# Kernel optimization log

Hardware: AMD Instinct MI355X
Metric: run time of the kernel (lower is better)

## Reference

```python
import jax, jax.numpy as jnp
import numpy as np

B, L = 4, 40960
C = 512
DMLP = 2048
TEMP = 1e-5
EPS = 1e-5
FACTOR = 2  # Smartpool factor at layer 4


def setup_inputs() -> dict:
    key = jax.random.key(0)
    ks = jax.random.split(key, 8)

    def w(k, shape, fan_in):
        return jax.random.normal(k, shape, jnp.float32) / np.float32(np.sqrt(fan_in))

    inp = {
        "x": jax.random.normal(ks[0], (B, 1, L), jnp.float32),
        "conv0_w": w(ks[1], (C, 1, 10), 10),   "conv0_b": jnp.zeros(C, jnp.float32),
        "conv1_w": w(ks[2], (C, C, 8), C * 8), "conv1_b": jnp.zeros(C, jnp.float32),
        "conv2_w": w(ks[3], (C, C, 4), C * 4), "conv2_b": jnp.zeros(C, jnp.float32),
        "conv3_w": w(ks[4], (C, C, 4), C * 4), "conv3_b": jnp.zeros(C, jnp.float32),
        "mlp_w1": w(ks[5], (C, DMLP), C),       "mlp_b1": jnp.zeros(DMLP, jnp.float32),
        "mlp_w2": w(ks[6], (DMLP, DMLP), DMLP), "mlp_b2": jnp.zeros(DMLP, jnp.float32),
        "mlp_w3": w(ks[7], (DMLP, 1), DMLP),    "mlp_b3": jnp.zeros(1, jnp.float32),
    }
    for i in range(5):  # ChannelNorm affine params (init: ones/zeros)
        inp[f"n{i}_w"] = jnp.ones(C, jnp.float32)
        inp[f"n{i}_b"] = jnp.zeros(C, jnp.float32)
    return inp


def _conv(x, w, b, stride, pad):
    # Conv1d with padding_mode='reflect': reflect-pad then VALID conv. x: [B,C,T]
    x = jnp.pad(x, ((0, 0), (0, 0), (pad, pad)), mode="reflect")
    y = jax.lax.conv_general_dilated(x, w, (stride,), "VALID",
                                     dimension_numbers=("NCH", "OIH", "NCH"))
    return y + b[None, :, None]


def _cnorm(x, g, b):
    # ChannelNorm: normalize over channel dim with unbiased variance (torch.var default)
    m = jnp.mean(x, axis=1, keepdims=True)
    v = jnp.var(x, axis=1, keepdims=True, ddof=1)
    return (x - m) * jax.lax.rsqrt(v + EPS) * g[None, :, None] + b[None, :, None]


def _forward(x, conv0_w, conv0_b, conv1_w, conv1_b, conv2_w, conv2_b, conv3_w, conv3_b,
             n0_w, n0_b, n1_w, n1_b, n2_w, n2_b, n3_w, n3_b, n4_w, n4_b,
             mlp_w1, mlp_b1, mlp_w2, mlp_b2, mlp_w3, mlp_b3):
    h = jax.nn.relu(_cnorm(_conv(x, conv0_w, conv0_b, 5, 3), n0_w, n0_b))
    h = jax.nn.relu(_cnorm(_conv(h, conv1_w, conv1_b, 4, 2), n1_w, n1_b))
    h = jax.nn.relu(_cnorm(_conv(h, conv2_w, conv2_b, 2, 1), n2_w, n2_b))
    h = jax.nn.relu(_cnorm(_conv(h, conv3_w, conv3_b, 2, 1), n3_w, n3_b))

    f = jnp.transpose(h, (0, 2, 1))  # [B,T,C]
    T = f.shape[1]

    # importance MLP (dropout inactive in eval), exact GELU, sigmoid head
    z = jax.nn.gelu(f @ mlp_w1 + mlp_b1, approximate=False)
    z = jax.nn.gelu(z @ mlp_w2 + mlp_b2, approximate=False)
    imp = jax.nn.sigmoid((z @ mlp_w3 + mlp_b3)[..., 0]) + TEMP          # [B,T]
    imp = imp / jnp.sum(imp, axis=1, keepdims=True) * (T / FACTOR)      # sums to T/factor

    # warp: cumsum -> ramp contributions -> 2x2 [[-1,1],[1,-1]] conv = double diff
    Tn = T // FACTOR  # == round(importance_cs[0,-1])
    cs = jnp.cumsum(imp, axis=1)                                        # [B,T]
    p = jnp.maximum(cs[:, :, None] - jnp.arange(Tn, dtype=cs.dtype)[None, None, :], 0.0)  # [B,T,Tn]
    pc = jnp.pad(p, ((0, 0), (0, 0), (0, 1)))
    d = pc[:, :, :-1] - pc[:, :, 1:]                                    # diff along new-time axis
    wmat = d - jnp.pad(d, ((0, 0), (1, 0), (0, 0)))[:, :-1, :]          # diff along old-time axis, [B,T,Tn]
    pooled = jnp.einsum("btn,btc->bnc", wmat, f)                        # interp_weights @ X

    out = jnp.transpose(pooled, (0, 2, 1))                              # [B,C,Tn]
    return jax.nn.relu(_cnorm(out, n4_w, n4_b))


def reference(x, conv0_w, conv0_b, conv1_w, conv1_b, conv2_w, conv2_b, conv3_w, conv3_b,
              n0_w, n0_b, n1_w, n1_b, n2_w, n2_b, n3_w, n3_b, n4_w, n4_b,
              mlp_w1, mlp_b1, mlp_w2, mlp_b2, mlp_w3, mlp_b3):
    return _forward(x, conv0_w, conv0_b, conv1_w, conv1_b, conv2_w, conv2_b, conv3_w, conv3_b,
                    n0_w, n0_b, n1_w, n1_b, n2_w, n2_b, n3_w, n3_b, n4_w, n4_b,
                    mlp_w1, mlp_b1, mlp_w2, mlp_b2, mlp_w3, mlp_b3)
```

## Files before the change

kernel.cpp:

```cpp
#include <hip/hip_runtime.h>
#include <hip/hip_bf16.h>
#include <math.h>

#define NB 4
#define LIN 40960
#define NC 512
#define T0 8192
#define T1 2048
#define T2 1024
#define T3 512
#define TN 256
#define DM 2048
#define EPSF 1e-5f
#define TEMPF 1e-5f

typedef __attribute__((ext_vector_type(8))) short bf16x8;
typedef __attribute__((ext_vector_type(4))) float f32x4;

__device__ __forceinline__ int refl(int t, int T) {
  if (t < 0) t = -t;
  if (t >= T) t = 2 * T - 2 - t;
  return t;
}

__device__ __forceinline__ void gld16(void* lds, const void* g) {
  __builtin_amdgcn_global_load_lds((const __attribute__((address_space(1))) unsigned int*)g,
                                   (__attribute__((address_space(3))) unsigned int*)lds, 16, 0, 0);
}

__device__ __forceinline__ void blk_sum2_512(float& a, float& b, float* scratch) {
#pragma unroll
  for (int off = 32; off > 0; off >>= 1) {
    a += __shfl_down(a, off, 64);
    b += __shfl_down(b, off, 64);
  }
  int lane = threadIdx.x & 63, wid = threadIdx.x >> 6;
  __syncthreads();
  if (lane == 0) { scratch[wid] = a; scratch[8 + wid] = b; }
  __syncthreads();
  float sa = 0.f, sb = 0.f;
#pragma unroll
  for (int i = 0; i < 8; i++) { sa += scratch[i]; sb += scratch[8 + i]; }
  a = sa; b = sb;
}

__device__ __forceinline__ void add_bf8(const __hip_bfloat16* p, float* v) {
  union { uint4 u; __hip_bfloat16 h[8]; } pk;
  pk.u = *(const uint4*)p;
#pragma unroll
  for (int j = 0; j < 8; j++) v[j] += __bfloat162float(pk.h[j]);
}

template <int KT>
__device__ __forceinline__ void prep_conv_body(const float* __restrict__ w, __hip_bfloat16* __restrict__ wt,
                                               int co, float* l) {
  const float* wb = w + (size_t)co * 512 * KT;
  for (int i = threadIdx.x; i < 512 * KT; i += 512) l[i] = wb[i];
  __syncthreads();
  __hip_bfloat16* wo = wt + (size_t)co * 512 * KT;
  for (int i = threadIdx.x; i < 512 * KT; i += 512) {
    int kk = i >> 9, ci = i & 511;
    wo[i] = __float2bfloat16(l[ci * KT + kk]);
  }
}

template <int KD, int ND>
__device__ __forceinline__ void prep_mlp_body(const float* __restrict__ w, __hip_bfloat16* __restrict__ wt,
                                              int bidx, float* sbuf) {
  float(*tile)[33] = (float(*)[33])sbuf;
  int bx = bidx % (ND / 32);
  int by = bidx / (ND / 32);
  int tx = threadIdx.x & 31, ty = threadIdx.x >> 5;
#pragma unroll
  for (int i = 0; i < 32; i += 16)
    tile[ty + i][tx] = w[(size_t)(by * 32 + ty + i) * ND + bx * 32 + tx];
  __syncthreads();
#pragma unroll
  for (int i = 0; i < 32; i += 16)
    wt[(size_t)(bx * 32 + ty + i) * KD + by * 32 + tx] = __float2bfloat16(tile[tx][ty + i]);
}

__device__ __forceinline__ void conv0_body(const float* __restrict__ x, const float* __restrict__ w,
                                           const float* __restrict__ bias, const float* __restrict__ gw,
                                           const float* __restrict__ gb, __hip_bfloat16* __restrict__ out,
                                           int blk, float* smem) {
  float* xv = smem;
  float* tb = smem + 64;
  float* stats = smem + 4672;
  int b = blk / (T0 / 8);
  int t0 = (blk % (T0 / 8)) * 8;
  int tid = threadIdx.x;
  if (tid < 45) xv[tid] = x[(size_t)b * LIN + refl(t0 * 5 - 3 + tid, LIN)];
  __syncthreads();
  float wk[10];
#pragma unroll
  for (int k = 0; k < 10; k++) wk[k] = w[tid * 10 + k];
  float bs = bias[tid];
  float acc[8];
#pragma unroll
  for (int tt = 0; tt < 8; tt++) {
    float a = bs;
#pragma unroll
    for (int k = 0; k < 10; k++) a += xv[tt * 5 + k] * wk[k];
    acc[tt] = a;
    tb[tid * 9 + tt] = a;
  }
  __syncthreads();
  int wave = tid >> 6, lane = tid & 63;
  float s = 0.f, q = 0.f;
#pragma unroll
  for (int j = 0; j < 8; j++) {
    float v = tb[(lane * 8 + j) * 9 + wave];
    s += v; q += v * v;
  }
#pragma unroll
  for (int off = 32; off > 0; off >>= 1) {
    s += __shfl_xor(s, off, 64);
    q += __shfl_xor(q, off, 64);
  }
  if (lane == 0) {
    float mean = s * (1.f / NC);
    float var = fmaxf((q - s * s * (1.f / NC)) * (1.f / (NC - 1)), 0.f);
    stats[wave] = mean;
    stats[8 + wave] = rsqrtf(var + EPSF);
  }
  __syncthreads();
  float gwv = gw[tid], gbv = gb[tid];
#pragma unroll
  for (int tt = 0; tt < 8; tt++) {
    float y = (acc[tt] - stats[tt]) * stats[8 + tt] * gwv + gbv;
    out[((size_t)(b * T0 + t0 + tt)) * NC + tid] = __float2bfloat16(fmaxf(y, 0.f));
  }
}

__global__ __launch_bounds__(512) void k_init(const float* x, const float* c0w, const float* c0b,
                                              const float* n0w, const float* n0b, __hip_bfloat16* h0b,
                                              const float* c1w, const float* c2w, const float* c3w,
                                              const float* mw1, const float* mw2,
                                              __hip_bfloat16* wt1, __hip_bfloat16* wt2,
                                              __hip_bfloat16* wt3, __hip_bfloat16* wm1t,
                                              __hip_bfloat16* wm2t) {
  __shared__ float smem[4688];
  int b = blockIdx.x;
  if (b < 4096) conv0_body(x, c0w, c0b, n0w, n0b, h0b, b, smem);
  else if (b < 4608) prep_conv_body<8>(c1w, wt1, b - 4096, smem);
  else if (b < 5120) prep_conv_body<4>(c2w, wt2, b - 4608, smem);
  else if (b < 5632) prep_conv_body<4>(c3w, wt3, b - 5120, smem);
  else if (b < 6656) prep_mlp_body<512, 2048>(mw1, wm1t, b - 5632, smem);
  else prep_mlp_body<2048, 2048>(mw2, wm2t, b - 6656, smem);
}

template <int MODE, int TIN_, int TOUT_, int SS, int PP, int KK, int NN, int SPLITK, int MM>
__global__ __launch_bounds__(512, 2) void k_gemmE(const __hip_bfloat16* __restrict__ A,
                                                  const __hip_bfloat16* __restrict__ Bt,
                                                  __hip_bfloat16* __restrict__ Cp) {
  __shared__ __align__(16) __hip_bfloat16 sA[2][2][256 * 32];
  __shared__ __align__(16) __hip_bfloat16 sB[2][2][256 * 32];
  const int tid = threadIdx.x;
  const int lane = tid & 63;
  const int wave = tid >> 6;
  const int wm = wave >> 2, wn = wave & 3;
  constexpr int nt = NN / 256;
  constexpr int PS = (MM / 2048) * nt;
  constexpr int KBT = KK / 32;
  constexpr int NT = KBT / (2 * SPLITK);
  const int blk = blockIdx.x;
  const int xs = blk & 7, sl = blk >> 3;
  const int sk = sl / PS, rem = sl % PS;
  const int row0 = ((rem / nt) * 8 + xs) * 256;
  const int col0 = (rem % nt) * 256;
  const int kb0 = sk * (KBT / SPLITK);
  const int cq = lane >> 4, cl = lane & 15;

  const char* aP[2];
  const char* bP[2];

  auto stageA = [&](int kb, int buf, int kk) {
    bool recalc = (kb == kb0) || (MODE == 1 && (kb & 15) == 0);
    if (recalc) {
#pragma unroll
      for (int rr = 0; rr < 2; rr++) {
        int c = rr * 512 + tid;
        int m = c >> 2, kc = c & 3;
        int kcs = kc ^ (m & 3);
        size_t ga;
        if (MODE == 0) {
          ga = (size_t)(row0 + m) * KK + kb * 32 + kcs * 8;
        } else {
          int r = row0 + m;
          int bb = r / TOUT_;
          int t = r - bb * TOUT_;
          int k = (kb * 32) >> 9;
          int ci = ((kb * 32) & 511) + kcs * 8;
          int gt = refl(t * SS - PP + k, TIN_);
          ga = (((size_t)(bb * TIN_ + gt)) << 9) + ci;
        }
        aP[rr] = (const char*)(A + ga);
      }
    }
#pragma unroll
    for (int rr = 0; rr < 2; rr++) {
      gld16((char*)&sA[buf][kk][0] + (rr * 512 + tid) * 16, aP[rr]);
      aP[rr] += 64;
    }
  };

  auto stageB = [&](int buf, int kk) {
#pragma unroll
    for (int rr = 0; rr < 2; rr++) {
      gld16((char*)&sB[buf][kk][0] + (rr * 512 + tid) * 16, bP[rr]);
      bP[rr] += 64;
    }
  };

#pragma unroll
  for (int rr = 0; rr < 2; rr++) {
    int c = rr * 512 + tid;
    int n = c >> 2, kc = c & 3;
    int kcs = kc ^ (n & 3);
    bP[rr] = (const char*)(Bt + (size_t)(col0 + n) * KK + kb0 * 32 + kcs * 8);
  }

  f32x4 acc[8][4];
  const f32x4 zz = {0.f, 0.f, 0.f, 0.f};
#pragma unroll
  for (int mi = 0; mi < 8; mi++)
#pragma unroll
    for (int ni = 0; ni < 4; ni++) acc[mi][ni] = zz;

  stageA(kb0, 0, 0);
  stageB(0, 0);
  stageA(kb0 + 1, 0, 1);
  stageB(0, 1);
  asm volatile("s_waitcnt vmcnt(0)" ::: "memory");
  __builtin_amdgcn_s_barrier();

  const int p = cq ^ (cl & 3);
  for (int t = 0; t < NT; ++t) {
    const int buf = t & 1;
    const int kbase = kb0 + 2 * t;
    const short* bA0 = (const short*)&sA[buf][0][0];
    const short* bA1 = (const short*)&sA[buf][1][0];
    const short* bB0 = (const short*)&sB[buf][0][0];
    const short* bB1 = (const short*)&sB[buf][1][0];
    bf16x8 bfr0[4], bfr1[4];
#pragma unroll
    for (int q = 0; q < 4; ++q) {
      bf16x8 af0[2], af1[2];
      if (q == 0) {
#pragma unroll
        for (int ni = 0; ni < 4; ni++) {
          bfr0[ni] = *(const bf16x8*)(bB0 + (wn * 64 + ni * 16 + cl) * 32 + p * 8);
          bfr1[ni] = *(const bf16x8*)(bB1 + (wn * 64 + ni * 16 + cl) * 32 + p * 8);
        }
      }
#pragma unroll
      for (int i = 0; i < 2; i++) {
        int mi = q * 2 + i;
        af0[i] = *(const bf16x8*)(bA0 + (wm * 128 + mi * 16 + cl) * 32 + p * 8);
        af1[i] = *(const bf16x8*)(bA1 + (wm * 128 + mi * 16 + cl) * 32 + p * 8);
      }
      if (t + 1 < NT) {
        if (q == 0) stageA(kbase + 2, buf ^ 1, 0);
        else if (q == 1) stageB(buf ^ 1, 0);
        else if (q == 2) stageA(kbase + 3, buf ^ 1, 1);
        else stageB(buf ^ 1, 1);
      }
      __builtin_amdgcn_s_barrier();
      asm volatile("s_waitcnt lgkmcnt(0)" ::: "memory");
      __builtin_amdgcn_s_setprio(1);
#pragma unroll
      for (int i = 0; i < 2; i++)
#pragma unroll
        for (int ni = 0; ni < 4; ni++) {
          acc[q * 2 + i][ni] =
              __builtin_amdgcn_mfma_f32_16x16x32_bf16(af0[i], bfr0[ni], acc[q * 2 + i][ni], 0, 0, 0);
          acc[q * 2 + i][ni] =
              __builtin_amdgcn_mfma_f32_16x16x32_bf16(af1[i], bfr1[ni], acc[q * 2 + i][ni], 0, 0, 0);
        }
      __builtin_amdgcn_s_setprio(0);
      if (q == 3 && t + 1 < NT) asm volatile("s_waitcnt vmcnt(0)" ::: "memory");
      __builtin_amdgcn_s_barrier();
    }
  }

#pragma unroll
  for (int mi = 0; mi < 8; mi++)
#pragma unroll
    for (int ni = 0; ni < 4; ni++)
#pragma unroll
      for (int r2 = 0; r2 < 4; r2++) {
        int row = row0 + wm * 128 + mi * 16 + cq * 4 + r2;
        int col = col0 + wn * 64 + ni * 16 + cl;
        Cp[(size_t)sk * MM * NN + (size_t)row * NN + col] = __float2bfloat16(acc[mi][ni][r2]);
      }
}

template <int MODE, int TIN_, int TOUT_, int SS, int PP, int KK, int NN, int SPLITK, int MM>
__global__ __launch_bounds__(256) void k_gemmB(const __hip_bfloat16* __restrict__ A,
                                               const __hip_bfloat16* __restrict__ Bt,
                                               __hip_bfloat16* __restrict__ Cp) {
  __shared__ __align__(16) __hip_bfloat16 sA[2][128 * 32];
  __shared__ __align__(16) __hip_bfloat16 sB[2][2][128 * 32];
  const int tid = threadIdx.x;
  const int lane = tid & 63;
  const int wave = tid >> 6;
  const int wm = wave >> 1, wn = wave & 1;
  constexpr int nt = NN / 128;
  constexpr int PS = (MM / 1024) * nt;
  constexpr int KBT = KK / 32;
  const int blk = blockIdx.x;
  const int xs = blk & 7, sl = blk >> 3;
  const int sk = sl / PS, rem = sl % PS;
  const int row0 = ((rem / nt) * 8 + xs) * 128;
  const int col0 = (rem % nt) * 128;
  const int kb0 = (sk * KBT) / SPLITK, kb1 = ((sk + 1) * KBT) / SPLITK;
  const int cq = lane >> 4, cl = lane & 15;

  const char* aP[2];
  const char* bP[2];

  auto stageA = [&](int kb, int buf) {
    bool recalc = (kb == kb0) || (MODE == 1 && (kb & 15) == 0);
    if (recalc) {
#pragma unroll
      for (int rr = 0; rr < 2; rr++) {
        int c = rr * 256 + tid;
        int m = c >> 2, kc = c & 3;
        int kcs = kc ^ (m & 3);
        size_t ga;
        if (MODE == 0) {
          ga = (size_t)(row0 + m) * KK + kb * 32 + kcs * 8;
        } else {
          int r = row0 + m;
          int bb = r / TOUT_;
          int t = r - bb * TOUT_;
          int k = (kb * 32) >> 9;
          int ci = ((kb * 32) & 511) + kcs * 8;
          int gt = refl(t * SS - PP + k, TIN_);
          ga = (((size_t)(bb * TIN_ + gt)) << 9) + ci;
        }
        aP[rr] = (const char*)(A + ga);
      }
    }
#pragma unroll
    for (int rr = 0; rr < 2; rr++) {
      gld16((char*)&sA[buf][0] + (rr * 256 + tid) * 16, aP[rr]);
      aP[rr] += 64;
    }
  };

  auto stageB = [&](int buf, bool doSub1) {
#pragma unroll
    for (int rr = 0; rr < 2; rr++) {
      gld16((char*)&sB[buf][0][0] + (rr * 256 + tid) * 16, bP[rr]);
      if (doSub1) gld16((char*)&sB[buf][1][0] + (rr * 256 + tid) * 16, bP[rr] + 64);
      bP[rr] += 128;
    }
  };

#pragma unroll
  for (int rr = 0; rr < 2; rr++) {
    int c = rr * 256 + tid;
    int n = c >> 2, kc = c & 3;
    int kcs = kc ^ (n & 3);
    bP[rr] = (const char*)(Bt + (size_t)(col0 + n) * KK + kb0 * 32 + kcs * 8);
  }

  f32x4 acc[4][4];
  const f32x4 zz = {0.f, 0.f, 0.f, 0.f};
#pragma unroll
  for (int mi = 0; mi < 4; mi++)
#pragma unroll
    for (int ni = 0; ni < 4; ni++) acc[mi][ni] = zz;

  stageA(kb0, 0);
  stageB(0, kb0 + 1 < kb1);

  const int p = cq ^ (cl & 3);
  for (int kb = kb0; kb < kb1; kb++) {
    const int jj = kb - kb0;
    __syncthreads();
    if (kb + 1 < kb1) stageA(kb + 1, (jj + 1) & 1);
    if (((jj & 1) == 0) && (kb + 2 < kb1)) stageB(((jj >> 1) + 1) & 1, kb + 3 < kb1);
    const short* bA = (const short*)&sA[jj & 1][0];
    const short* bB = (const short*)&sB[(jj >> 1) & 1][jj & 1][0];
    bf16x8 af[4], bfr[4];
#pragma unroll
    for (int mi = 0; mi < 4; mi++)
      af[mi] = *(const bf16x8*)(bA + (wm * 64 + mi * 16 + cl) * 32 + p * 8);
#pragma unroll
    for (int ni = 0; ni < 4; ni++)
      bfr[ni] = *(const bf16x8*)(bB + (wn * 64 + ni * 16 + cl) * 32 + p * 8);
#pragma unroll
    for (int mi = 0; mi < 4; mi++)
#pragma unroll
      for (int ni = 0; ni < 4; ni++)
        acc[mi][ni] = __builtin_amdgcn_mfma_f32_16x16x32_bf16(af[mi], bfr[ni], acc[mi][ni], 0, 0, 0);
  }

#pragma unroll
  for (int mi = 0; mi < 4; mi++)
#pragma unroll
    for (int ni = 0; ni < 4; ni++)
#pragma unroll
      for (int r2 = 0; r2 < 4; r2++) {
        int row = row0 + wm * 64 + mi * 16 + cq * 4 + r2;
        int col = col0 + wn * 64 + ni * 16 + cl;
        Cp[(size_t)sk * MM * NN + (size_t)row * NN + col] = __float2bfloat16(acc[mi][ni][r2]);
      }
}

template <int MODE, int TIN_, int TOUT_, int SS, int PP, int KK, int NN, int EPI, int SPLITK, int MM>
__global__ __launch_bounds__(256, 4) void k_gemmC(const __hip_bfloat16* __restrict__ A,
                                                  const __hip_bfloat16* __restrict__ Bt,
                                                  const float* __restrict__ bias,
                                                  __hip_bfloat16* __restrict__ Cout) {
  __shared__ __align__(16) __hip_bfloat16 sA[2][64 * 32];
  __shared__ __align__(16) __hip_bfloat16 sB[2][2][128 * 32];
  const int tid = threadIdx.x;
  const int lane = tid & 63;
  const int wave = tid >> 6;
  const int wm = wave >> 1, wn = wave & 1;
  constexpr int nt = NN / 128;
  constexpr int PS = (MM / 512) * nt;
  constexpr int KBT = KK / 32;
  const int blk = blockIdx.x;
  const int xs = blk & 7, sl = blk >> 3;
  const int sk = sl / PS, rem = sl % PS;
  const int row0 = ((rem / nt) * 8 + xs) * 64;
  const int col0 = (rem % nt) * 128;
  const int kb0 = (sk * KBT) / SPLITK, kb1 = ((sk + 1) * KBT) / SPLITK;
  const int cq = lane >> 4, cl = lane & 15;

  const char* aP;
  const char* bP[2];

  auto stageA = [&](int kb, int buf) {
    bool recalc = (kb == kb0) || (MODE == 1 && (kb & 15) == 0);
    if (recalc) {
      int m = tid >> 2, kc = tid & 3;
      int kcs = kc ^ (m & 3);
      size_t ga;
      if (MODE == 0) {
        ga = (size_t)(row0 + m) * KK + kb * 32 + kcs * 8;
      } else {
        int r = row0 + m;
        int bb = r / TOUT_;
        int t = r - bb * TOUT_;
        int k = (kb * 32) >> 9;
        int ci = ((kb * 32) & 511) + kcs * 8;
        int gt = refl(t * SS - PP + k, TIN_);
        ga = (((size_t)(bb * TIN_ + gt)) << 9) + ci;
      }
      aP = (const char*)(A + ga);
    }
    gld16((char*)&sA[buf][0] + tid * 16, aP);
    aP += 64;
  };

  auto stageB = [&](int buf, bool doSub1) {
#pragma unroll
    for (int rr = 0; rr < 2; rr++) {
      gld16((char*)&sB[buf][0][0] + (rr * 256 + tid) * 16, bP[rr]);
      if (doSub1) gld16((char*)&sB[buf][1][0] + (rr * 256 + tid) * 16, bP[rr] + 64);
      bP[rr] += 128;
    }
  };

#pragma unroll
  for (int rr = 0; rr < 2; rr++) {
    int c = rr * 256 + tid;
    int n = c >> 2, kc = c & 3;
    int kcs = kc ^ (n & 3);
    bP[rr] = (const char*)(Bt + (size_t)(col0 + n) * KK + kb0 * 32 + kcs * 8);
  }

  f32x4 acc[2][4];
  const f32x4 zz = {0.f, 0.f, 0.f, 0.f};
#pragma unroll
  for (int mi = 0; mi < 2; mi++)
#pragma unroll
    for (int ni = 0; ni < 4; ni++) acc[mi][ni] = zz;

  stageA(kb0, 0);
  stageB(0, kb0 + 1 < kb1);

  const int p = cq ^ (cl & 3);
  for (int kb = kb0; kb < kb1; kb++) {
    const int jj = kb - kb0;
    __syncthreads();
    if (kb + 1 < kb1) stageA(kb + 1, (jj + 1) & 1);
    if (((jj & 1) == 0) && (kb + 2 < kb1)) stageB(((jj >> 1) + 1) & 1, kb + 3 < kb1);
    const short* bA = (const short*)&sA[jj & 1][0];
    const short* bB = (const short*)&sB[(jj >> 1) & 1][jj & 1][0];
    bf16x8 af[2], bfr[4];
#pragma unroll
    for (int mi = 0; mi < 2; mi++)
      af[mi] = *(const bf16x8*)(bA + (wm * 32 + mi * 16 + cl) * 32 + p * 8);
#pragma unroll
    for (int ni = 0; ni < 4; ni++)
      bfr[ni] = *(const bf16x8*)(bB + (wn * 64 + ni * 16 + cl) * 32 + p * 8);
#pragma unroll
    for (int mi = 0; mi < 2; mi++)
#pragma unroll
      for (int ni = 0; ni < 4; ni++)
        acc[mi][ni] = __builtin_amdgcn_mfma_f32_16x16x32_bf16(af[mi], bfr[ni], acc[mi][ni], 0, 0, 0);
  }

#pragma unroll
  for (int mi = 0; mi < 2; mi++)
#pragma unroll
    for (int ni = 0; ni < 4; ni++)
#pragma unroll
      for (int r2 = 0; r2 < 4; r2++) {
        int row = row0 + wm * 32 + mi * 16 + cq * 4 + r2;
        int col = col0 + wn * 64 + ni * 16 + cl;
        float v = acc[mi][ni][r2];
        if (EPI == 1) {
          v += bias[col];
          v = 0.5f * v * (1.f + erff(v * 0.70710678118654752f));
          Cout[(size_t)row * NN + col] = __float2bfloat16(v);
        } else {
          Cout[(size_t)sk * MM * NN + (size_t)row * NN + col] = __float2bfloat16(v);
        }
      }
}

template <int NS>
__global__ __launch_bounds__(512) void k_cnorm(const __hip_bfloat16* __restrict__ g,
                                               const float* __restrict__ cb,
                                               const float* __restrict__ gw, const float* __restrict__ gb,
                                               __hip_bfloat16* __restrict__ out, size_t stride) {
  int wave = threadIdx.x >> 6, lane = threadIdx.x & 63;
  size_t row = (size_t)blockIdx.x * 8 + wave;
  float v[8];
  {
    float4 c0 = *(const float4*)(cb + lane * 8), c1 = *(const float4*)(cb + lane * 8 + 4);
    v[0] = c0.x; v[1] = c0.y; v[2] = c0.z; v[3] = c0.w;
    v[4] = c1.x; v[5] = c1.y; v[6] = c1.z; v[7] = c1.w;
  }
#pragma unroll
  for (int s = 0; s < NS; s++) add_bf8(g + s * stride + row * NC + lane * 8, v);
  float s = 0.f, q = 0.f;
#pragma unroll
  for (int j = 0; j < 8; j++) { s += v[j]; q += v[j] * v[j]; }
#pragma unroll
  for (int off = 32; off > 0; off >>= 1) {
    s += __shfl_xor(s, off, 64);
    q += __shfl_xor(q, off, 64);
  }
  float mean = s * (1.f / NC);
  float var = fmaxf((q - s * s * (1.f / NC)) * (1.f / (NC - 1)), 0.f);
  float rstd = rsqrtf(var + EPSF);
  float4 w0 = *(const float4*)(gw + lane * 8), w1 = *(const float4*)(gw + lane * 8 + 4);
  float4 b0 = *(const float4*)(gb + lane * 8), b1 = *(const float4*)(gb + lane * 8 + 4);
  float gwv[8] = {w0.x, w0.y, w0.z, w0.w, w1.x, w1.y, w1.z, w1.w};
  float gbv[8] = {b0.x, b0.y, b0.z, b0.w, b1.x, b1.y, b1.z, b1.w};
  union { __hip_bfloat16 h[8]; uint4 u; } pk;
#pragma unroll
  for (int j = 0; j < 8; j++)
    pk.h[j] = __float2bfloat16(fmaxf((v[j] - mean) * rstd * gwv[j] + gbv[j], 0.f));
  *(uint4*)(out + row * NC + lane * 8) = pk.u;
}

template <int NS>
__global__ __launch_bounds__(256) void k_head(const __hip_bfloat16* __restrict__ g,
                                              const float* __restrict__ b2,
                                              const float* __restrict__ w3, const float* __restrict__ b3,
                                              float* __restrict__ imp) {
  __shared__ float red[4];
  int row = blockIdx.x, tid = threadIdx.x;
  int c = tid * 8;
  float v[8];
  {
    float4 x0 = *(const float4*)(b2 + c), x1 = *(const float4*)(b2 + c + 4);
    v[0] = x0.x; v[1] = x0.y; v[2] = x0.z; v[3] = x0.w;
    v[4] = x1.x; v[5] = x1.y; v[6] = x1.z; v[7] = x1.w;
  }
#pragma unroll
  for (int s = 0; s < NS; s++) add_bf8(g + (size_t)s * (2048 * DM) + (size_t)row * DM + c, v);
  float a = 0.f;
  float4 w0 = *(const float4*)(w3 + c), w1 = *(const float4*)(w3 + c + 4);
  float wv[8] = {w0.x, w0.y, w0.z, w0.w, w1.x, w1.y, w1.z, w1.w};
#pragma unroll
  for (int j = 0; j < 8; j++) {
    float z = 0.5f * v[j] * (1.f + erff(v[j] * 0.70710678118654752f));
    a += z * wv[j];
  }
#pragma unroll
  for (int off = 32; off > 0; off >>= 1) a += __shfl_down(a, off, 64);
  int lane = tid & 63, wid = tid >> 6;
  if (lane == 0) red[wid] = a;
  __syncthreads();
  if (tid == 0) {
    float s = red[0] + red[1] + red[2] + red[3] + b3[0];
    imp[row] = 1.f / (1.f + expf(-s)) + TEMPF;
  }
}

__device__ __forceinline__ float dfun(float cv, int n) {
  float d = fmaxf(cv - (float)n, 0.f);
  if (n < TN - 1) d = fminf(d, 1.f);
  return d;
}

__global__ __launch_bounds__(512) void k_poolfinal(const __hip_bfloat16* __restrict__ f,
                                                   const float* __restrict__ imp,
                                                   const float* __restrict__ gw, const float* __restrict__ gb,
                                                   float* __restrict__ out) {
  __shared__ float wt[T3];
  __shared__ float wsum[8];
  __shared__ float red[16];
  int b = blockIdx.x / TN, n = blockIdx.x % TN;
  int tid = threadIdx.x, wave = tid >> 6, lane = tid & 63;
  float own = imp[b * T3 + tid];
  float s = own;
#pragma unroll
  for (int off = 1; off < 64; off <<= 1) {
    float t = __shfl_up(s, off, 64);
    if (lane >= off) s += t;
  }
  if (lane == 63) wsum[wave] = s;
  __syncthreads();
  float prefix = 0.f, total = 0.f;
#pragma unroll
  for (int w = 0; w < 8; w++) {
    float ws_ = wsum[w];
    total += ws_;
    if (w < wave) prefix += ws_;
  }
  float scale = (float)TN / total;
  float incl = (prefix + s) * scale;
  float excl = (prefix + s - own) * scale;
  wt[tid] = dfun(incl, n) - dfun(excl, n);
  __syncthreads();
  float acc = 0.f;
  for (int t = 0; t < T3; t++) {
    float w = wt[t];
    if (w != 0.f) acc += w * __bfloat162float(f[((size_t)b * T3 + t) * NC + tid]);
  }
  float sv = acc, q = acc * acc;
  blk_sum2_512(sv, q, red);
  float mean = sv * (1.f / NC);
  float var = fmaxf((q - sv * sv * (1.f / NC)) * (1.f / (NC - 1)), 0.f);
  float y = (acc - mean) * rsqrtf(var + EPSF) * gw[tid] + gb[tid];
  out[((size_t)b * NC + tid) * TN + n] = fmaxf(y, 0.f);
}

extern "C" void kernel_launch(void* const* d_in, const int* in_sizes, int n_in,
                              void* d_out, int out_size, void* d_ws, size_t ws_size,
                              hipStream_t stream) {
  const float* x   = (const float*)d_in[0];
  const float* c0w = (const float*)d_in[1];  const float* c0b = (const float*)d_in[2];
  const float* c1w = (const float*)d_in[3];  const float* c1b = (const float*)d_in[4];
  const float* c2w = (const float*)d_in[5];  const float* c2b = (const float*)d_in[6];
  const float* c3w = (const float*)d_in[7];  const float* c3b = (const float*)d_in[8];
  const float* mw1 = (const float*)d_in[9];  const float* mb1 = (const float*)d_in[10];
  const float* mw2 = (const float*)d_in[11]; const float* mb2 = (const float*)d_in[12];
  const float* mw3 = (const float*)d_in[13]; const float* mb3 = (const float*)d_in[14];
  const float* n0w = (const float*)d_in[15]; const float* n0b = (const float*)d_in[16];
  const float* n1w = (const float*)d_in[17]; const float* n1b = (const float*)d_in[18];
  const float* n2w = (const float*)d_in[19]; const float* n2b = (const float*)d_in[20];
  const float* n3w = (const float*)d_in[21]; const float* n3b = (const float*)d_in[22];
  const float* n4w = (const float*)d_in[23]; const float* n4b = (const float*)d_in[24];

  char* base = (char*)d_ws;
  __hip_bfloat16* h0b  = (__hip_bfloat16*)(base);
  __hip_bfloat16* h1b  = (__hip_bfloat16*)(base);
  __hip_bfloat16* h2b  = (__hip_bfloat16*)(base + (8u << 20));
  __hip_bfloat16* h3b  = (__hip_bfloat16*)(base + (12u << 20));
  __hip_bfloat16* z1b  = (__hip_bfloat16*)(base + (14u << 20));
  float*          imp  = (float*)(base + (22u << 20));
  __hip_bfloat16* g    = (__hip_bfloat16*)(base + (32u << 20));
  __hip_bfloat16* wm1t = (__hip_bfloat16*)(base + (64u << 20));
  __hip_bfloat16* wt2  = (__hip_bfloat16*)(base + (66u << 20));
  __hip_bfloat16* wt3  = (__hip_bfloat16*)(base + (68u << 20));
  __hip_bfloat16* wt1  = (__hip_bfloat16*)(base + (70u << 20));
  __hip_bfloat16* wm2t = (__hip_bfloat16*)(base + (74u << 20));
  float* outp = (float*)d_out;

  k_init<<<4096 + 6656, 512, 0, stream>>>(x, c0w, c0b, n0w, n0b, h0b,
                                          c1w, c2w, c3w, mw1, mw2, wt1, wt2, wt3, wm1t, wm2t);

  k_gemmE<1, 8192, 2048, 4, 2, 4096, 512, 4, 8192><<<256, 512, 0, stream>>>(h0b, wt1, g);
  k_cnorm<4><<<8192 / 8, 512, 0, stream>>>(g, c1b, n1w, n1b, h1b, (size_t)8192 * 512);
  k_gemmB<1, 2048, 1024, 2, 1, 2048, 512, 6, 4096><<<768, 256, 0, stream>>>(h1b, wt2, g);
  k_cnorm<6><<<4096 / 8, 512, 0, stream>>>(g, c2b, n2w, n2b, h2b, (size_t)4096 * 512);
  k_gemmC<1, 1024, 512, 2, 1, 2048, 512, 0, 6, 2048><<<768, 256, 0, stream>>>(h2b, wt3, c3b, g);
  k_cnorm<6><<<2048 / 8, 512, 0, stream>>>(g, c3b, n3w, n3b, h3b, (size_t)2048 * 512);
  k_gemmC<0, 0, 1, 0, 0, 512, 2048, 1, 1, 2048><<<512, 256, 0, stream>>>(h3b, wm1t, mb1, z1b);
  k_gemmE<0, 0, 1, 0, 0, 2048, 2048, 4, 2048><<<256, 512, 0, stream>>>(z1b, wm2t, g);

  k_head<4><<<NB * T3, 256, 0, stream>>>(g, mb2, mw3, mb3, imp);
  k_poolfinal<<<NB * TN, 512, 0, stream>>>(h3b, imp, n4w, n4b, outp);
}
```

Before: 326.5 us.

## Replace double-buffered GEMM loop with 4-slot ring buffer prefetching three K-steps ahead

Restructures the big GEMM kernel so shared memory holds four 32-wide K slices in a ring instead of two double-buffered pairs. Global loads are issued three K-steps ahead, and the wait is a partial vmcnt rather than draining all outstanding loads each iteration. This aims to hide global memory latency better and avoid the full vmcnt(0) stall. The cost is more barriers per K step, more A-fragment LDS reads per step, and a per-step loop structure whose waits must exactly match the number of outstanding loads.

```diff
diff --git a/kernel.cpp b/kernel.cpp
--- a/kernel.cpp
+++ b/kernel.cpp
@@ -151,11 +151,11 @@
 }
 
 template <int MODE, int TIN_, int TOUT_, int SS, int PP, int KK, int NN, int SPLITK, int MM>
-__global__ __launch_bounds__(512, 2) void k_gemmE(const __hip_bfloat16* __restrict__ A,
+__global__ __launch_bounds__(512, 2) void k_gemmF(const __hip_bfloat16* __restrict__ A,
                                                   const __hip_bfloat16* __restrict__ Bt,
                                                   __hip_bfloat16* __restrict__ Cp) {
-  __shared__ __align__(16) __hip_bfloat16 sA[2][2][256 * 32];
-  __shared__ __align__(16) __hip_bfloat16 sB[2][2][256 * 32];
+  __shared__ __align__(16) __hip_bfloat16 sA[4][256 * 32];
+  __shared__ __align__(16) __hip_bfloat16 sB[4][256 * 32];
   const int tid = threadIdx.x;
   const int lane = tid & 63;
   const int wave = tid >> 6;
@@ -163,19 +163,19 @@
   constexpr int nt = NN / 256;
   constexpr int PS = (MM / 2048) * nt;
   constexpr int KBT = KK / 32;
-  constexpr int NT = KBT / (2 * SPLITK);
+  constexpr int NS = KBT / SPLITK;
   const int blk = blockIdx.x;
   const int xs = blk & 7, sl = blk >> 3;
   const int sk = sl / PS, rem = sl % PS;
   const int row0 = ((rem / nt) * 8 + xs) * 256;
   const int col0 = (rem % nt) * 256;
-  const int kb0 = sk * (KBT / SPLITK);
+  const int kb0 = sk * NS;
   const int cq = lane >> 4, cl = lane & 15;
 
   const char* aP[2];
   const char* bP[2];
 
-  auto stageA = [&](int kb, int buf, int kk) {
+  auto stageA = [&](int kb, int slot) {
     bool recalc = (kb == kb0) || (MODE == 1 && (kb & 15) == 0);
     if (recalc) {
 #pragma unroll
@@ -200,15 +200,15 @@
     }
 #pragma unroll
     for (int rr = 0; rr < 2; rr++) {
-      gld16((char*)&sA[buf][kk][0] + (rr * 512 + tid) * 16, aP[rr]);
+      gld16((char*)&sA[slot][0] + (rr * 512 + tid) * 16, aP[rr]);
       aP[rr] += 64;
     }
   };
 
-  auto stageB = [&](int buf, int kk) {
+  auto stageB = [&](int slot) {
 #pragma unroll
     for (int rr = 0; rr < 2; rr++) {
-      gld16((char*)&sB[buf][kk][0] + (rr * 512 + tid) * 16, bP[rr]);
+      gld16((char*)&sB[slot][0] + (rr * 512 + tid) * 16, bP[rr]);
       bP[rr] += 64;
     }
   };
@@ -228,60 +228,58 @@
 #pragma unroll
     for (int ni = 0; ni < 4; ni++) acc[mi][ni] = zz;
 
-  stageA(kb0, 0, 0);
-  stageB(0, 0);
-  stageA(kb0 + 1, 0, 1);
-  stageB(0, 1);
-  asm volatile("s_waitcnt vmcnt(0)" ::: "memory");
+  stageA(kb0 + 0, 0); stageB(0);
+  if (NS > 1) { stageA(kb0 + 1, 1); stageB(1); }
+  if (NS > 2) { stageA(kb0 + 2, 2); stageB(2); }
+  if (NS > 2)      { asm volatile("s_waitcnt vmcnt(8)" ::: "memory"); }
+  else if (NS > 1) { asm volatile("s_waitcnt vmcnt(4)" ::: "memory"); }
+  else             { asm volatile("s_waitcnt vmcnt(0)" ::: "memory"); }
   __builtin_amdgcn_s_barrier();
 
   const int p = cq ^ (cl & 3);
-  for (int t = 0; t < NT; ++t) {
-    const int buf = t & 1;
-    const int kbase = kb0 + 2 * t;
-    const short* bA0 = (const short*)&sA[buf][0][0];
-    const short* bA1 = (const short*)&sA[buf][1][0];
-    const short* bB0 = (const short*)&sB[buf][0][0];
-    const short* bB1 = (const short*)&sB[buf][1][0];
-    bf16x8 bfr0[4], bfr1[4];
-#pragma unroll
-    for (int q = 0; q < 4; ++q) {
-      bf16x8 af0[2], af1[2];
-      if (q == 0) {
-#pragma unroll
-        for (int ni = 0; ni < 4; ni++) {
-          bfr0[ni] = *(const bf16x8*)(bB0 + (wn * 64 + ni * 16 + cl) * 32 + p * 8);
-          bfr1[ni] = *(const bf16x8*)(bB1 + (wn * 64 + ni * 16 + cl) * 32 + p * 8);
-        }
-      }
-#pragma unroll
-      for (int i = 0; i < 2; i++) {
-        int mi = q * 2 + i;
-        af0[i] = *(const bf16x8*)(bA0 + (wm * 128 + mi * 16 + cl) * 32 + p * 8);
-        af1[i] = *(const bf16x8*)(bA1 + (wm * 128 + mi * 16 + cl) * 32 + p * 8);
-      }
-      if (t + 1 < NT) {
-        if (q == 0) stageA(kbase + 2, buf ^ 1, 0);
-        else if (q == 1) stageB(buf ^ 1, 0);
-        else if (q == 2) stageA(kbase + 3, buf ^ 1, 1);
-        else stageB(buf ^ 1, 1);
-      }
-      __builtin_amdgcn_s_barrier();
-      asm volatile("s_waitcnt lgkmcnt(0)" ::: "memory");
-      __builtin_amdgcn_s_setprio(1);
-#pragma unroll
-      for (int i = 0; i < 2; i++)
-#pragma unroll
-        for (int ni = 0; ni < 4; ni++) {
-          acc[q * 2 + i][ni] =
-              __builtin_amdgcn_mfma_f32_16x16x32_bf16(af0[i], bfr0[ni], acc[q * 2 + i][ni], 0, 0, 0);
-          acc[q * 2 + i][ni] =
-              __builtin_amdgcn_mfma_f32_16x16x32_bf16(af1[i], bfr1[ni], acc[q * 2 + i][ni], 0, 0, 0);
-        }
-      __builtin_amdgcn_s_setprio(0);
-      if (q == 3 && t + 1 < NT) asm volatile("s_waitcnt vmcnt(0)" ::: "memory");
-      __builtin_amdgcn_s_barrier();
-    }
+  for (int s = 0; s < NS; ++s) {
+    const int slot = s & 3;
+    const short* bA = (const short*)&sA[slot][0];
+    const short* bB = (const short*)&sB[slot][0];
+    bf16x8 bfr[4], af[4];
+
+#pragma unroll
+    for (int ni = 0; ni < 4; ni++)
+      bfr[ni] = *(const bf16x8*)(bB + (wn * 64 + ni * 16 + cl) * 32 + p * 8);
+#pragma unroll
+    for (int i = 0; i < 4; i++)
+      af[i] = *(const bf16x8*)(bA + (wm * 128 + i * 16 + cl) * 32 + p * 8);
+    if (s + 3 < NS) stageA(kb0 + s + 3, (s + 3) & 3);
+    __builtin_amdgcn_s_barrier();
+    asm volatile("s_waitcnt lgkmcnt(0)" ::: "memory");
+    __builtin_amdgcn_s_setprio(1);
+#pragma unroll
+    for (int i = 0; i < 4; i++)
+#pragma unroll
+      for (int ni = 0; ni < 4; ni++)
+        acc[i][ni] = __builtin_amdgcn_mfma_f32_16x16x32_bf16(af[i], bfr[ni], acc[i][ni], 0, 0, 0);
+    __builtin_amdgcn_s_setprio(0);
+    __builtin_amdgcn_s_barrier();
+
+#pragma unroll
+    for (int i = 0; i < 4; i++)
+      af[i] = *(const bf16x8*)(bA + (wm * 128 + (4 + i) * 16 + cl) * 32 + p * 8);
+    if (s + 3 < NS) stageB((s + 3) & 3);
+    if (s + 1 < NS) {
+      if (s + 3 < NS)      { asm volatile("s_waitcnt vmcnt(8)" ::: "memory"); }
+      else if (s + 2 < NS) { asm volatile("s_waitcnt vmcnt(4)" ::: "memory"); }
+      else                 { asm volatile("s_waitcnt vmcnt(0)" ::: "memory"); }
+    }
+    __builtin_amdgcn_s_barrier();
+    asm volatile("s_waitcnt lgkmcnt(0)" ::: "memory");
+    __builtin_amdgcn_s_setprio(1);
+#pragma unroll
+    for (int i = 0; i < 4; i++)
+#pragma unroll
+      for (int ni = 0; ni < 4; ni++)
+        acc[4 + i][ni] = __builtin_amdgcn_mfma_f32_16x16x32_bf16(af[i], bfr[ni], acc[4 + i][ni], 0, 0, 0);
+    __builtin_amdgcn_s_setprio(0);
+    __builtin_amdgcn_s_barrier();
   }
 
 #pragma unroll
@@ -683,14 +681,14 @@
   k_init<<<4096 + 6656, 512, 0, stream>>>(x, c0w, c0b, n0w, n0b, h0b,
                                           c1w, c2w, c3w, mw1, mw2, wt1, wt2, wt3, wm1t, wm2t);
 
-  k_gemmE<1, 8192, 2048, 4, 2, 4096, 512, 4, 8192><<<256, 512, 0, stream>>>(h0b, wt1, g);
+  k_gemmF<1, 8192, 2048, 4, 2, 4096, 512, 4, 8192><<<256, 512, 0, stream>>>(h0b, wt1, g);
   k_cnorm<4><<<8192 / 8, 512, 0, stream>>>(g, c1b, n1w, n1b, h1b, (size_t)8192 * 512);
   k_gemmB<1, 2048, 1024, 2, 1, 2048, 512, 6, 4096><<<768, 256, 0, stream>>>(h1b, wt2, g);
   k_cnorm<6><<<4096 / 8, 512, 0, stream>>>(g, c2b, n2w, n2b, h2b, (size_t)4096 * 512);
   k_gemmC<1, 1024, 512, 2, 1, 2048, 512, 0, 6, 2048><<<768, 256, 0, stream>>>(h2b, wt3, c3b, g);
   k_cnorm<6><<<2048 / 8, 512, 0, stream>>>(g, c3b, n3w, n3b, h3b, (size_t)2048 * 512);
   k_gemmC<0, 0, 1, 0, 0, 512, 2048, 1, 1, 2048><<<512, 256, 0, stream>>>(h3b, wm1t, mb1, z1b);
-  k_gemmE<0, 0, 1, 0, 0, 2048, 2048, 4, 2048><<<256, 512, 0, stream>>>(z1b, wm2t, g);
+  k_gemmF<0, 0, 1, 0, 0, 2048, 2048, 4, 2048><<<256, 512, 0, stream>>>(z1b, wm2t, g);
 
   k_head<4><<<NB * T3, 256, 0, stream>>>(g, mb2, mw3, mb3, imp);
   k_poolfinal<<<NB * TN, 512, 0, stream>>>(h3b, imp, n4w, n4b, outp);
```

After: 319.1 us. 1.02x faster.
